# Kernel tuning notes

Measured on AMD Instinct MI355X. Metric: run time of the kernel, lower is better.

Reference implementation:

```python
import jax, jax.numpy as jnp
import numpy as np

GAMMA = 0.5
BATCH, DIM, UNITS = 16384, 512, 1024


def setup_inputs() -> dict:
    key = jax.random.key(0)
    k1, k2 = jax.random.split(key)
    inputs = jax.random.normal(k1, (BATCH, DIM), dtype=jnp.float32)
    mu = jax.random.normal(k2, (DIM, UNITS), dtype=jnp.float32)
    return {"inputs": inputs, "mu": mu}


def reference(inputs, mu):
    # Squared L2 distance from each input row to each center (column of mu):
    x_sq = jnp.sum(inputs * inputs, axis=1, keepdims=True)        # [B, 1]
    mu_sq = jnp.sum(mu * mu, axis=0, keepdims=True)               # [1, U]
    cross = inputs @ mu                                           # [B, U] GEMM
    l2 = x_sq - 2.0 * cross + mu_sq                                # [B, U]
    return jnp.exp(-GAMMA * l2)
```

## Files before the change

### kernel.cpp

```cpp
#include <hip/hip_runtime.h>

#define BATCH 16384
#define DIM   512
#define UNITS 1024

typedef float v16f __attribute__((ext_vector_type(16)));

#define BPITCH 33
#define MFMA_F8(a, b, c) __builtin_amdgcn_mfma_f32_32x32x16_fp8_fp8((a), (b), (c), 0, 0, 0)

static __device__ __forceinline__ int2 cvt8(const float4 f0, const float4 f1) {
    int lo = __builtin_amdgcn_cvt_pk_fp8_f32(f0.x, f0.y, 0, false);
    lo     = __builtin_amdgcn_cvt_pk_fp8_f32(f0.z, f0.w, lo, true);
    int hi = __builtin_amdgcn_cvt_pk_fp8_f32(f1.x, f1.y, 0, false);
    hi     = __builtin_amdgcn_cvt_pk_fp8_f32(f1.z, f1.w, hi, true);
    return make_int2(lo, hi);
}
static __device__ __forceinline__ float dot8(const float4 f0, const float4 f1) {
    return f0.x * f0.x + f0.y * f0.y + f0.z * f0.z + f0.w * f0.w
         + f1.x * f1.x + f1.y * f1.y + f1.z * f1.z + f1.w * f1.w;
}

__global__ __launch_bounds__(256)
void prep_b_kernel(const float* __restrict__ mu, unsigned char* __restrict__ B8f,
                   float* __restrict__ musq) {
    __shared__ __attribute__((aligned(16))) char smem[512 * BPITCH * 4 + 1024];
    float* lds = (float*)smem;
    float* red = (float*)(smem + 512 * BPITCH * 4);
    const int t  = threadIdx.x;
    const int l  = t & 63, w = t >> 6;
    const int ln = l & 31, h = l >> 5;
    const int nb = blockIdx.x;
    const int n0 = nb * 32;
    const int col = t & 31, kg = t >> 5;
    float s = 0.f;
    for (int i = 0; i < 64; i++) {
        const int k = i * 8 + kg;
        float v = mu[(size_t)k * UNITS + n0 + col];
        s += v * v;
        lds[k * BPITCH + col] = v;
    }
    red[col * 8 + kg] = s;
    __syncthreads();
    if (t < 32) {
        float a = 0.f;
#pragma unroll
        for (int i = 0; i < 8; i++) a += red[t * 8 + i];
        musq[n0 + t] = a;
    }
#pragma unroll
    for (int j = 0; j < 8; j++) {
        const int kw = w * 8 + j;
        const float* p = lds + (kw * 16 + h * 8) * BPITCH + ln;
        float f[8];
#pragma unroll
        for (int i = 0; i < 8; i++) f[i] = p[i * BPITCH];
        *(int2*)(B8f + (((size_t)nb * 32 + kw) * 64 + l) * 8) =
            cvt8(make_float4(f[0], f[1], f[2], f[3]),
                 make_float4(f[4], f[5], f[6], f[7]));
    }
}

__global__ __launch_bounds__(1024, 4)
void rbf_main_kernel(const float* __restrict__ in,
                     const unsigned char* __restrict__ B8f,
                     const float* __restrict__ musq,
                     float* __restrict__ out) {
    __shared__ __attribute__((aligned(16))) unsigned char smem[107520];
    float* stage = (float*)smem;
    unsigned char* Afrag = smem + 66048;
    float* red   = (float*)(smem + 98816);
    float* xsq_l = (float*)(smem + 107264);

    const int t  = threadIdx.x;
    const int l  = t & 63;
    const int w  = t >> 6;
    const int ln = l & 31;
    const int h  = l >> 5;
    const int m0 = blockIdx.x * 64;

#pragma unroll
    for (int rc = 0; rc < 2; rc++) {
        const float4* src = (const float4*)(in + (size_t)(m0 + rc * 32) * DIM);
        float4* s4 = (float4*)stage;
#pragma unroll
        for (int i = 0; i < 4; i++) {
            const int f = i * 1024 + t;
            s4[(f >> 7) * 129 + (f & 127)] = src[f];
        }
        __syncthreads();
        float s = 0.f;
#pragma unroll
        for (int j = 0; j < 2; j++) {
            const int kw = w * 2 + j;
            const float* p = stage + ln * 516 + kw * 16 + h * 8;
            float4 f0 = *(const float4*)p;
            float4 f1 = *(const float4*)(p + 4);
            s += dot8(f0, f1);
            *(int2*)(Afrag + (((rc * 32 + kw) * 64) + h * 32 + ln) * 8) =
                cvt8(f0, f1);
        }
        red[(rc * 32 + ln) * 33 + w * 2 + h] = s;
        __syncthreads();
    }
    if (t < 64) {
        float a = 0.f;
#pragma unroll
        for (int i = 0; i < 32; i++) a += red[t * 33 + i];
        xsq_l[t] = -0.5f * a;
    }
    __syncthreads();

    const int wr = w >> 3;
    const int wc = w & 7;
    const long* Af = (const long*)(Afrag + (size_t)wr * 16384);
    const long* Bg = (const long*)B8f + (size_t)(wc * 4) * 2048 + l;
    const size_t mrow = m0 + wr * 32;

#pragma unroll
    for (int g2 = 0; g2 < 2; g2++) {
        const long* B0 = Bg + (size_t)(g2 * 2) * 2048;
        const long* B1 = B0 + 2048;

        v16f acc0 = (v16f)0.f, acc1 = (v16f)0.f;
#pragma unroll 8
        for (int kw = 0; kw < 32; kw++) {
            long a  = Af[kw * 64 + l];
            long b0 = B0[kw * 64];
            long b1 = B1[kw * 64];
            acc0 = MFMA_F8(a, b0, acc0);
            acc1 = MFMA_F8(a, b1, acc1);
        }

        const int nc0 = wc * 128 + g2 * 64;
        const float mb0 = -0.5f * musq[nc0 + ln];
        const float mb1 = -0.5f * musq[nc0 + 32 + ln];
        float* obase = out + nc0 + ln;
#pragma unroll
        for (int r = 0; r < 16; r++) {
            const int rl = (r & 3) + 8 * (r >> 2) + 4 * h;
            const float xb = xsq_l[wr * 32 + rl];
            float* orow = obase + (mrow + rl) * UNITS;
            __builtin_nontemporal_store(__expf(acc0[r] + xb + mb0), orow);
            __builtin_nontemporal_store(__expf(acc1[r] + xb + mb1), orow + 32);
        }
    }
}

extern "C" void kernel_launch(void* const* d_in, const int* in_sizes, int n_in,
                              void* d_out, int out_size, void* d_ws, size_t ws_size,
                              hipStream_t stream) {
    const float* inputs = (const float*)d_in[0];
    const float* mu     = (const float*)d_in[1];
    float* out = (float*)d_out;

    char* ws = (char*)d_ws;
    unsigned char* B8f = (unsigned char*)ws;
    float* musq = (float*)(ws + (size_t)UNITS * DIM);

    prep_b_kernel<<<32, 256, 0, stream>>>(mu, B8f, musq);
    rbf_main_kernel<<<256, 1024, 0, stream>>>(inputs, B8f, musq, out);
}
```

Before: 107.7 us.

## Halve main-kernel block to 32 rows and 512 threads, doubling grid

The main kernel now processes 32 input rows per block with 8 waves instead of 64 rows with 16 waves, and launches 512 blocks instead of 256. LDS use drops to about half and the staging/conversion phase is remapped so each thread handles two k-chunks for one row. This spreads work over more blocks to fill all CUs and improve occupancy and latency hiding, at the cost of each B fragment being loaded from global/L2 twice as often overall.

```diff
diff --git a/kernel.cpp b/kernel.cpp
--- a/kernel.cpp
+++ b/kernel.cpp
@@ -61,49 +61,49 @@
     }
 }
 
-__global__ __launch_bounds__(1024, 4)
+__global__ __launch_bounds__(512, 4)
 void rbf_main_kernel(const float* __restrict__ in,
                      const unsigned char* __restrict__ B8f,
                      const float* __restrict__ musq,
                      float* __restrict__ out) {
-    __shared__ __attribute__((aligned(16))) unsigned char smem[107520];
+    __shared__ __attribute__((aligned(16))) unsigned char smem[53760];
     float* stage = (float*)smem;
-    unsigned char* Afrag = smem + 66048;
-    float* red   = (float*)(smem + 98816);
-    float* xsq_l = (float*)(smem + 107264);
+    unsigned char* Afrag = smem + 33024;
+    float* red   = (float*)(smem + 49408);
+    float* xsq_l = (float*)(smem + 53632);
 
     const int t  = threadIdx.x;
     const int l  = t & 63;
     const int w  = t >> 6;
     const int ln = l & 31;
     const int h  = l >> 5;
-    const int m0 = blockIdx.x * 64;
+    const int m0 = blockIdx.x * 32;
 
 #pragma unroll
-    for (int rc = 0; rc < 2; rc++) {
-        const float4* src = (const float4*)(in + (size_t)(m0 + rc * 32) * DIM);
+    for (int s = 0; s < 2; s++) {
+        const float4* src = (const float4*)(in + (size_t)(m0 + s * 16) * DIM);
         float4* s4 = (float4*)stage;
 #pragma unroll
         for (int i = 0; i < 4; i++) {
-            const int f = i * 1024 + t;
+            const int f = i * 512 + t;
             s4[(f >> 7) * 129 + (f & 127)] = src[f];
         }
         __syncthreads();
-        float s = 0.f;
-#pragma unroll
-        for (int j = 0; j < 2; j++) {
-            const int kw = w * 2 + j;
-            const float* p = stage + ln * 516 + kw * 16 + h * 8;
-            float4 f0 = *(const float4*)p;
-            float4 f1 = *(const float4*)(p + 4);
-            s += dot8(f0, f1);
-            *(int2*)(Afrag + (((rc * 32 + kw) * 64) + h * 32 + ln) * 8) =
-                cvt8(f0, f1);
-        }
-        red[(rc * 32 + ln) * 33 + w * 2 + h] = s;
+        const int row  = t & 15;
+        const int slot = t >> 4;
+        const int hh   = slot & 1, kw = slot >> 1;
+        const int rg   = s * 16 + row;
+        const float* p = stage + row * 516 + kw * 16 + hh * 8;
+        float4 a0 = *(const float4*)p;
+        float4 a1 = *(const float4*)(p + 4);
+        float4 b0 = *(const float4*)(p + 256);
+        float4 b1 = *(const float4*)(p + 260);
+        red[rg * 33 + slot] = dot8(a0, a1) + dot8(b0, b1);
+        *(int2*)(Afrag + ((kw * 64) + hh * 32 + rg) * 8)        = cvt8(a0, a1);
+        *(int2*)(Afrag + (((kw + 16) * 64) + hh * 32 + rg) * 8) = cvt8(b0, b1);
         __syncthreads();
     }
-    if (t < 64) {
+    if (t < 32) {
         float a = 0.f;
 #pragma unroll
         for (int i = 0; i < 32; i++) a += red[t * 33 + i];
@@ -111,11 +111,8 @@
     }
     __syncthreads();
 
-    const int wr = w >> 3;
-    const int wc = w & 7;
-    const long* Af = (const long*)(Afrag + (size_t)wr * 16384);
-    const long* Bg = (const long*)B8f + (size_t)(wc * 4) * 2048 + l;
-    const size_t mrow = m0 + wr * 32;
+    const long* Af = (const long*)Afrag;
+    const long* Bg = (const long*)B8f + (size_t)(w * 4) * 2048 + l;
 
 #pragma unroll
     for (int g2 = 0; g2 < 2; g2++) {
@@ -132,15 +129,15 @@
             acc1 = MFMA_F8(a, b1, acc1);
         }
 
-        const int nc0 = wc * 128 + g2 * 64;
+        const int nc0 = w * 128 + g2 * 64;
         const float mb0 = -0.5f * musq[nc0 + ln];
         const float mb1 = -0.5f * musq[nc0 + 32 + ln];
         float* obase = out + nc0 + ln;
 #pragma unroll
         for (int r = 0; r < 16; r++) {
             const int rl = (r & 3) + 8 * (r >> 2) + 4 * h;
-            const float xb = xsq_l[wr * 32 + rl];
-            float* orow = obase + (mrow + rl) * UNITS;
+            const float xb = xsq_l[rl];
+            float* orow = obase + (size_t)(m0 + rl) * UNITS;
             __builtin_nontemporal_store(__expf(acc0[r] + xb + mb0), orow);
             __builtin_nontemporal_store(__expf(acc1[r] + xb + mb1), orow + 32);
         }
@@ -159,5 +156,5 @@
     float* musq = (float*)(ws + (size_t)UNITS * DIM);
 
     prep_b_kernel<<<32, 256, 0, stream>>>(mu, B8f, musq);
-    rbf_main_kernel<<<256, 1024, 0, stream>>>(inputs, B8f, musq, out);
+    rbf_main_kernel<<<512, 512, 0, stream>>>(inputs, B8f, musq, out);
 }
```

Result: slower. 116.2 us (+7.9%).
